# Performance work log

Hardware: AMD Instinct MI355X
Metric: run time of the kernel (lower is better)

The kernel has to match this reference:

```python
import math
import jax, jax.numpy as jnp
import numpy as np

N_NODES = 50000
N_EDGES = 600000
D = 128          # in_dim == out_dim
T = 4            # num_types
R = 4            # num_relations
H = 8            # n_heads
DK = D // H
MAX_LEN = 240    # RelTemporalEncoding max_len
EPS = 1e-5


def _sinusoid_table(n_hid, max_len):
    pos = jnp.arange(max_len, dtype=jnp.float32)[:, None]
    div = jnp.exp(jnp.arange(0, n_hid, 2, dtype=jnp.float32) * (-math.log(10000.0) / n_hid))
    s = jnp.sin(pos * div) / math.sqrt(n_hid)
    c = jnp.cos(pos * div) / math.sqrt(n_hid)
    emb = jnp.zeros((max_len, n_hid), dtype=jnp.float32)
    emb = emb.at[:, 0::2].set(s).at[:, 1::2].set(c)
    return emb


def setup_inputs() -> dict:
    key = jax.random.key(0)
    ks = jax.random.split(key, 24)
    f32 = jnp.float32
    inp = {
        'node_inp': jax.random.normal(ks[0], (N_NODES, D), dtype=f32),
        'node_type': jax.random.randint(ks[1], (N_NODES,), 0, T),
        'edge_index': jax.random.randint(ks[2], (2, N_EDGES), 0, N_NODES),
        'edge_type': jax.random.randint(ks[3], (N_EDGES,), 0, R),
        'edge_time': jax.random.randint(ks[4], (N_EDGES,), 0, MAX_LEN),
        # per-type Linear weights stored as [T, in, out] (x @ W + b)
        'Wk': jax.random.normal(ks[5], (T, D, D), dtype=f32) * 0.05,
        'bk': jnp.zeros((T, D), dtype=f32),
        'Wq': jax.random.normal(ks[6], (T, D, D), dtype=f32) * 0.05,
        'bq': jnp.zeros((T, D), dtype=f32),
        'Wv': jax.random.normal(ks[7], (T, D, D), dtype=f32) * 0.05,
        'bv': jnp.zeros((T, D), dtype=f32),
        'Wa': jax.random.normal(ks[8], (T, D, D), dtype=f32) * 0.05,
        'ba': jnp.zeros((T, D), dtype=f32),
        'gamma': jnp.ones((T, D), dtype=f32),
        'beta': jnp.zeros((T, D), dtype=f32),
        'rel_pri': jnp.ones((R, H), dtype=f32),
        'rel_att': jax.random.normal(ks[9], (R, H, DK, DK), dtype=f32) * 0.1,
        'rel_msg': jax.random.normal(ks[10], (R, H, DK, DK), dtype=f32) * 0.1,
        'skip': jnp.ones((T,), dtype=f32),
        'rte_W': jax.random.normal(ks[11], (D, D), dtype=f32) * 0.05,
        'rte_b': jnp.zeros((D,), dtype=f32),
    }
    return inp


def _type_proj(x, W, b, types):
    # all-type projection [T, N, D] then gather per-node type (T is small)
    allp = jnp.einsum('ni,tio->tno', x, W) + b[:, None, :]
    return allp[types, jnp.arange(x.shape[0])]


def reference(node_inp, node_type, edge_index, edge_type, edge_time,
              Wk, bk, Wq, bq, Wv, bv, Wa, ba, gamma, beta,
              rel_pri, rel_att, rel_msg, skip, rte_W, rte_b):
    N = node_inp.shape[0]
    E = edge_index.shape[1]
    src, tgt = edge_index[0], edge_index[1]  # j (source) -> i (target)

    # --- RelTemporalEncoding: x + Linear(emb[t]); emb is a fixed sinusoid table
    rte_out = _sinusoid_table(D, MAX_LEN) @ rte_W + rte_b  # [240, D]

    # --- per-node type-specific K/Q/V (linearity: K_t(x + rte) = K_t(x) + rte @ Wk_t)
    k_node = _type_proj(node_inp, Wk, bk, node_type)  # [N, D]
    v_node = _type_proj(node_inp, Wv, bv, node_type)
    q_node = _type_proj(node_inp, Wq, bq, node_type)
    k_rte = jnp.einsum('mi,tio->tmo', rte_out, Wk)  # [T, 240, D] (no bias; already in k_node)
    v_rte = jnp.einsum('mi,tio->tmo', rte_out, Wv)

    stype = node_type[src]
    k_e = (k_node[src] + k_rte[stype, edge_time]).reshape(E, H, DK)
    v_e = (v_node[src] + v_rte[stype, edge_time]).reshape(E, H, DK)
    q_e = q_node[tgt].reshape(E, H, DK)

    # --- per-relation head-wise transforms (R is small, fixed loop)
    k2 = jnp.zeros_like(k_e)
    msg = jnp.zeros_like(v_e)
    for r in range(R):
        sel = (edge_type == r)[:, None, None]
        k2 = jnp.where(sel, jnp.einsum('ehk,hkd->ehd', k_e, rel_att[r]), k2)
        msg = jnp.where(sel, jnp.einsum('ehk,hkd->ehd', v_e, rel_msg[r]), msg)

    logits = (q_e * k2).sum(-1) * rel_pri[edge_type] / math.sqrt(DK)  # [E, H]

    # --- softmax over edges grouped by target node
    m = jax.ops.segment_max(logits, tgt, num_segments=N)
    ex = jnp.exp(logits - m[tgt])
    den = jax.ops.segment_sum(ex, tgt, num_segments=N)
    att = ex / den[tgt]  # [E, H]

    res = (msg * att[..., None]).reshape(E, D)
    aggr = jax.ops.segment_sum(res, tgt, num_segments=N)  # [N, D]

    # --- update: per-type FFN + gated skip + per-type LayerNorm
    a = jax.nn.gelu(aggr, approximate=False)
    trans = _type_proj(a, Wa, ba, node_type)  # dropout p used in eval mode -> identity
    alpha = jax.nn.sigmoid(skip)[node_type][:, None]
    h = trans * alpha + node_inp * (1.0 - alpha)
    mu = h.mean(-1, keepdims=True)
    var = ((h - mu) ** 2).mean(-1, keepdims=True)
    out = (h - mu) / jnp.sqrt(var + EPS) * gamma[node_type] + beta[node_type]
    return out
```

## Files before the change

### kernel.cpp

```cpp
#include <hip/hip_runtime.h>
#include <math.h>

#define NH 8
#define NT 4
#define NR 4
#define MAXLEN 240

typedef __attribute__((ext_vector_type(8))) short bf16x8;
typedef __attribute__((ext_vector_type(4))) float f32x4;

__device__ __forceinline__ unsigned short f2bf(float x) {
    unsigned u = __float_as_uint(x);
    u += 0x7fffu + ((u >> 16) & 1u);
    return (unsigned short)(u >> 16);
}
__device__ __forceinline__ float bflo(unsigned u) { return __uint_as_float(u << 16); }
__device__ __forceinline__ float bfhi(unsigned u) { return __uint_as_float(u & 0xffff0000u); }
__device__ __forceinline__ unsigned pack2(float a, float b) {
    return (unsigned)f2bf(a) | ((unsigned)f2bf(b) << 16);
}
__device__ __forceinline__ float dp3(uint4 a, uint4 b, uint4 c) {
    return (bflo(a.x) + bflo(b.x)) * bflo(c.x) + (bfhi(a.x) + bfhi(b.x)) * bfhi(c.x)
         + (bflo(a.y) + bflo(b.y)) * bflo(c.y) + (bfhi(a.y) + bfhi(b.y)) * bfhi(c.y)
         + (bflo(a.z) + bflo(b.z)) * bflo(c.z) + (bfhi(a.z) + bfhi(b.z)) * bfhi(c.z)
         + (bflo(a.w) + bflo(b.w)) * bflo(c.w) + (bfhi(a.w) + bfhi(b.w)) * bfhi(c.w);
}

__global__ void zero_kernel(int* deg, int* cursor, int* dcnt, int* dcur, int N) {
    int i = blockIdx.x * blockDim.x + threadIdx.x;
    int stride = gridDim.x * blockDim.x;
    if (i < 256) { dcnt[i] = 0; dcur[i] = 0; }
    for (int j = i; j < N; j += stride) { deg[j] = 0; cursor[j] = 0; }
}

__global__ void deg_kernel(const int* __restrict__ ei, int* __restrict__ deg, int E) {
    int i = blockIdx.x * blockDim.x + threadIdx.x;
    int stride = gridDim.x * blockDim.x;
    for (int e = i; e < E; e += stride) atomicAdd(&deg[ei[E + e]], 1);
}

__global__ __launch_bounds__(256) void histA(const int* __restrict__ ntype,
                                             const int* __restrict__ deg,
                                             int* __restrict__ dcnt, int N) {
    __shared__ int h[256];
    int tid = threadIdx.x;
    h[tid] = 0;
    __syncthreads();
    int i = blockIdx.x * 256 + tid;
    if (i < N) atomicAdd(&h[ntype[i] * 64 + 63 - min(deg[i], 63)], 1);
    __syncthreads();
    if (h[tid]) atomicAdd(&dcnt[tid], h[tid]);
}

__global__ __launch_bounds__(256) void histB(const int* __restrict__ dcnt,
                                             int* __restrict__ dbase) {
    __shared__ int tmp[256];
    int v = dcnt[threadIdx.x];
    tmp[threadIdx.x] = v;
    __syncthreads();
    #pragma unroll
    for (int off = 1; off < 256; off <<= 1) {
        int t = threadIdx.x >= off ? tmp[threadIdx.x - off] : 0;
        __syncthreads();
        tmp[threadIdx.x] += t;
        __syncthreads();
    }
    dbase[threadIdx.x] = tmp[threadIdx.x] - v;
}

__global__ __launch_bounds__(256) void histC(const int* __restrict__ ntype,
                                             const int* __restrict__ deg,
                                             const int* __restrict__ dbase, int* __restrict__ dcur,
                                             int* __restrict__ nlist, int* __restrict__ spos,
                                             int* __restrict__ stype_s, int* __restrict__ deg_s,
                                             int N) {
    __shared__ int h[256];
    __shared__ int bb[256];
    __shared__ int cur[256];
    int tid = threadIdx.x;
    h[tid] = 0; cur[tid] = 0;
    __syncthreads();
    int i = blockIdx.x * 256 + tid;
    int b = -1, t = 0, dg = 0;
    if (i < N) {
        t = ntype[i]; dg = deg[i];
        b = t * 64 + 63 - min(dg, 63);
        atomicAdd(&h[b], 1);
    }
    __syncthreads();
    if (h[tid]) bb[tid] = atomicAdd(&dcur[tid], h[tid]);
    __syncthreads();
    if (i < N) {
        int r = atomicAdd(&cur[b], 1);
        int p = dbase[b] + bb[b] + r;
        nlist[p] = i;
        spos[i] = p;
        stype_s[p] = t;
        deg_s[p] = dg;
    }
}

__global__ __launch_bounds__(256) void scanA(const int* __restrict__ deg, int* __restrict__ excl,
                                             int* __restrict__ bsum, int N) {
    __shared__ int tmp[256];
    int i = blockIdx.x * 256 + threadIdx.x;
    int v = i < N ? deg[i] : 0;
    tmp[threadIdx.x] = v;
    __syncthreads();
    #pragma unroll
    for (int off = 1; off < 256; off <<= 1) {
        int t = threadIdx.x >= off ? tmp[threadIdx.x - off] : 0;
        __syncthreads();
        tmp[threadIdx.x] += t;
        __syncthreads();
    }
    if (i < N) excl[i] = tmp[threadIdx.x] - v;
    if (threadIdx.x == 255) bsum[blockIdx.x] = tmp[255];
}

__global__ __launch_bounds__(256) void scanB(int* __restrict__ bsum, int nb) {
    __shared__ int tmp[256];
    int v = threadIdx.x < nb ? bsum[threadIdx.x] : 0;
    tmp[threadIdx.x] = v;
    __syncthreads();
    #pragma unroll
    for (int off = 1; off < 256; off <<= 1) {
        int t = threadIdx.x >= off ? tmp[threadIdx.x - off] : 0;
        __syncthreads();
        tmp[threadIdx.x] += t;
        __syncthreads();
    }
    if (threadIdx.x < nb) bsum[threadIdx.x] = tmp[threadIdx.x] - v;
}

__global__ void scanC(const int* __restrict__ excl, const int* __restrict__ bsum,
                      int* __restrict__ row_start, int N) {
    int i = blockIdx.x * blockDim.x + threadIdx.x;
    if (i < N) row_start[i] = excl[i] + bsum[i >> 8];
}

__global__ void scatter_kernel(const int* __restrict__ ei, const int* __restrict__ etype,
                               const int* __restrict__ etime, const int* __restrict__ spos,
                               const int* __restrict__ dbase,
                               const int* __restrict__ row_start, int* __restrict__ cursor,
                               unsigned* __restrict__ ebuf, int E) {
    int tb1 = dbase[64], tb2 = dbase[128], tb3 = dbase[192];
    int i = blockIdx.x * blockDim.x + threadIdx.x;
    int stride = gridDim.x * blockDim.x;
    for (int e = i; e < E; e += stride) {
        int sps = spos[ei[e]];
        int spt = spos[ei[E + e]];
        int st = (sps >= tb1) + (sps >= tb2) + (sps >= tb3);
        int pos = atomicAdd(&cursor[spt], 1);
        ebuf[row_start[spt] + pos] =
            (unsigned)sps | ((unsigned)etype[e] << 17) | ((unsigned)etime[e] << 19) | ((unsigned)st << 27);
    }
}

__global__ __launch_bounds__(128) void rte_tables(
    const float* __restrict__ rte_W, const float* __restrict__ rte_b,
    const float* __restrict__ Wk, const float* __restrict__ Wv,
    const float* __restrict__ rel_msg,
    unsigned short* __restrict__ krte_bf, unsigned short* __restrict__ vmrte_bf) {
    int m = blockIdx.x, t = blockIdx.y, d = threadIdx.x;
    __shared__ float emb[128];
    __shared__ float sr[128];
    __shared__ float vr[128];
    int j2 = d & ~1;
    float div = expf((float)j2 * (-9.210340371976184f / 128.f));
    float ang = (float)m * div;
    emb[d] = ((d & 1) ? cosf(ang) : sinf(ang)) * 0.08838834764831845f;
    __syncthreads();
    float ro = rte_b[d];
    #pragma unroll 8
    for (int i = 0; i < 128; ++i) ro += emb[i] * rte_W[i * 128 + d];
    sr[d] = ro;
    __syncthreads();
    float ak = 0.f, av = 0.f;
    for (int i = 0; i < 128; ++i) {
        float rv = sr[i];
        ak += rv * Wk[(t * 128 + i) * 128 + d];
        av += rv * Wv[(t * 128 + i) * 128 + d];
    }
    krte_bf[(size_t)(t * MAXLEN + m) * 128 + d] = f2bf(ak);
    vr[d] = av;
    __syncthreads();
    int h = d >> 4, dd = d & 15;
    for (int r = 0; r < NR; ++r) {
        float acc = 0.f;
        #pragma unroll
        for (int k = 0; k < 16; ++k)
            acc += vr[h * 16 + k] * rel_msg[((r * NH + h) * 16 + k) * 16 + dd];
        vmrte_bf[(size_t)((t * 4 + r) * MAXLEN + m) * 128 + d] = f2bf(acc);
    }
}

__global__ __launch_bounds__(256) void pack_w9(
    const float* __restrict__ Wk, const float* __restrict__ Wq,
    const float* __restrict__ Wv, const float* __restrict__ Wa,
    const float* __restrict__ bk, const float* __restrict__ bq,
    const float* __restrict__ bv, const float* __restrict__ ba,
    const float* __restrict__ rel_att, const float* __restrict__ rel_msg,
    const float* __restrict__ rel_pri,
    short* __restrict__ PW2, float* __restrict__ PB) {
    if (blockIdx.x >= 320) {
        int bidx = (blockIdx.x - 320) * 256 + threadIdx.x;
        int col = bidx & 127, t = (bidx >> 7) & 3, set = bidx >> 9;
        int h = col >> 4, kk = col & 15;
        float val;
        if (set == 0) val = bk[t * 128 + col];
        else if (set == 9) val = ba[t * 128 + col];
        else if (set <= 4) {
            int r = set - 1;
            float pri = rel_pri[r * NH + h] * 0.25f;
            float acc = 0.f;
            #pragma unroll
            for (int dp = 0; dp < 16; ++dp)
                acc += bq[t * 128 + h * 16 + dp] * rel_att[((r * NH + h) * 16 + kk) * 16 + dp];
            val = acc * pri;
        } else {
            int r = set - 5;
            float acc = 0.f;
            #pragma unroll
            for (int kp = 0; kp < 16; ++kp)
                acc += bv[t * 128 + h * 16 + kp] * rel_msg[((r * NH + h) * 16 + kp) * 16 + kk];
            val = acc;
        }
        PB[bidx] = val;
        return;
    }
    int idx = blockIdx.x * 256 + threadIdx.x;
    int lane = idx & 63;
    int ks = (idx >> 6) & 3;
    int ctg = (idx >> 8) & 7;
    int t = (idx >> 11) & 3;
    int set = idx >> 13;
    int col = ctg * 16 + (lane & 15);
    int k0 = ks * 32 + (lane >> 4) * 8;
    int h = col >> 4, kk = col & 15;
    unsigned short o[8];
    if (set == 0 || set == 9) {
        const float* W = (set == 0 ? Wk : Wa) + t * 16384;
        #pragma unroll
        for (int j = 0; j < 8; ++j) o[j] = f2bf(W[(k0 + j) * 128 + col]);
    } else if (set <= 4) {
        int r = set - 1;
        float pri = rel_pri[r * NH + h] * 0.25f;
        float Ar[16];
        #pragma unroll
        for (int dp = 0; dp < 16; ++dp)
            Ar[dp] = rel_att[((r * NH + h) * 16 + kk) * 16 + dp] * pri;
        #pragma unroll
        for (int j = 0; j < 8; ++j) {
            const float* wr = Wq + (size_t)(t * 128 + k0 + j) * 128 + h * 16;
            float acc = 0.f;
            #pragma unroll
            for (int dp = 0; dp < 16; ++dp) acc += wr[dp] * Ar[dp];
            o[j] = f2bf(acc);
        }
    } else {
        int r = set - 5;
        float Mc[16];
        #pragma unroll
        for (int kp = 0; kp < 16; ++kp)
            Mc[kp] = rel_msg[((r * NH + h) * 16 + kp) * 16 + kk];
        #pragma unroll
        for (int j = 0; j < 8; ++j) {
            const float* wr = Wv + (size_t)(t * 128 + k0 + j) * 128 + h * 16;
            float acc = 0.f;
            #pragma unroll
            for (int kp = 0; kp < 16; ++kp) acc += wr[kp] * Mc[kp];
            o[j] = f2bf(acc);
        }
    }
    uint4 pk;
    pk.x = (unsigned)o[0] | ((unsigned)o[1] << 16);
    pk.y = (unsigned)o[2] | ((unsigned)o[3] << 16);
    pk.z = (unsigned)o[4] | ((unsigned)o[5] << 16);
    pk.w = (unsigned)o[6] | ((unsigned)o[7] << 16);
    *reinterpret_cast<uint4*>(PW2 + (size_t)idx * 8) = pk;
}

__global__ __launch_bounds__(256, 4) void kqv2(
    const float* __restrict__ x, const int* __restrict__ nlist_,
    const int* __restrict__ stype_s, const short* __restrict__ PW2,
    const float* __restrict__ PB,
    unsigned short* __restrict__ kn_s, unsigned short* __restrict__ qa_s,
    unsigned short* __restrict__ vm_s, int N) {
    __shared__ short af_l[2][4][64][8];
    __shared__ unsigned short ob[32][128];
    __shared__ int st_l[32];
    const int tid = threadIdx.x;
    const int sp0 = blockIdx.x * 32;
    if (tid < 32) {
        int sp = sp0 + tid;
        st_l[tid] = stype_s[sp < N ? sp : N - 1];
    }
    {
        int i = tid >> 3;
        int d0 = (tid & 7) * 16;
        int sp = sp0 + i;
        int nid = nlist_[sp < N ? sp : N - 1];
        const float* xr = x + (size_t)nid * 128 + d0;
        float4 f0 = *reinterpret_cast<const float4*>(xr);
        float4 f1 = *reinterpret_cast<const float4*>(xr + 4);
        float4 f2 = *reinterpret_cast<const float4*>(xr + 8);
        float4 f3 = *reinterpret_cast<const float4*>(xr + 12);
        int m = i >> 4, rr = i & 15;
        int ks = d0 >> 5;
        int sub = (d0 >> 3) & 3;
        uint4 p0, p1;
        p0.x = pack2(f0.x, f0.y); p0.y = pack2(f0.z, f0.w);
        p0.z = pack2(f1.x, f1.y); p0.w = pack2(f1.z, f1.w);
        p1.x = pack2(f2.x, f2.y); p1.y = pack2(f2.z, f2.w);
        p1.z = pack2(f3.x, f3.y); p1.w = pack2(f3.z, f3.w);
        *reinterpret_cast<uint4*>(&af_l[m][ks][sub * 16 + rr][0]) = p0;
        *reinterpret_cast<uint4*>(&af_l[m][ks][(sub + 1) * 16 + rr][0]) = p1;
    }
    __syncthreads();

    const int lane = tid & 63, w = tid >> 6;
    const int col_l = lane & 15, rowg = lane >> 4;
    const int t0 = st_l[0], t1 = st_l[31];

    bf16x8 afr[2][4];
    #pragma unroll
    for (int m = 0; m < 2; ++m)
        #pragma unroll
        for (int ks = 0; ks < 4; ++ks)
            afr[m][ks] = *reinterpret_cast<const bf16x8*>(&af_l[m][ks][lane][0]);

    for (int set = 0; set < 9; ++set) {
        for (int t = t0; t <= t1; ++t) {
            #pragma unroll
            for (int c = 0; c < 2; ++c) {
                int ctg = w + c * 4;
                bf16x8 pf[4];
                #pragma unroll
                for (int ks = 0; ks < 4; ++ks)
                    pf[ks] = *reinterpret_cast<const bf16x8*>(
                        PW2 + ((size_t)((((set * 4 + t) * 8 + ctg) * 4 + ks) * 64 + lane)) * 8);
                float bval = PB[(set * 4 + t) * 128 + ctg * 16 + col_l];
                #pragma unroll
                for (int m = 0; m < 2; ++m) {
                    f32x4 acc = {0.f, 0.f, 0.f, 0.f};
                    #pragma unroll
                    for (int ks = 0; ks < 4; ++ks)
                        acc = __builtin_amdgcn_mfma_f32_16x16x32_bf16(afr[m][ks], pf[ks], acc, 0, 0, 0);
                    #pragma unroll
                    for (int j = 0; j < 4; ++j) {
                        int i = m * 16 + rowg * 4 + j;
                        if (st_l[i] == t)
                            ob[i][ctg * 16 + col_l] = f2bf(acc[j] + bval);
                    }
                }
            }
        }
        __syncthreads();
        {
            int i = tid >> 3, d0 = (tid & 7) * 16;
            int sp = sp0 + i;
            if (sp < N) {
                unsigned short* dst;
                if (set == 0) dst = kn_s + (size_t)sp * 128;
                else if (set <= 4) dst = qa_s + ((size_t)sp * 4 + (set - 1)) * 128;
                else dst = vm_s + ((size_t)sp * 4 + (set - 5)) * 128;
                *reinterpret_cast<uint4*>(dst + d0) = *reinterpret_cast<const uint4*>(&ob[i][d0]);
                *reinterpret_cast<uint4*>(dst + d0 + 8) = *reinterpret_cast<const uint4*>(&ob[i][d0 + 8]);
            }
        }
        __syncthreads();
    }
}

__global__ __launch_bounds__(256) void fused_edge_attn(
    const unsigned* __restrict__ ebuf, const int* __restrict__ row_start,
    const int* __restrict__ deg_s,
    const unsigned short* __restrict__ kn_s, const unsigned short* __restrict__ krte_bf,
    const unsigned short* __restrict__ qa_s, const unsigned short* __restrict__ vm_s,
    const unsigned short* __restrict__ vmrte_bf,
    float* __restrict__ aggr, int N) {
    int sp = blockIdx.x * 16 + (threadIdx.x >> 4);
    int l16 = threadIdx.x & 15;
    if (sp >= N) return;
    uint4 q[4];
    #pragma unroll
    for (int r = 0; r < 4; ++r)
        q[r] = *reinterpret_cast<const uint4*>(qa_s + ((size_t)sp * 4 + r) * 128 + l16 * 8);
    int start = row_start[sp], cnt = deg_s[sp];
    float den = 0.f;
    float acc[8] = {0.f, 0.f, 0.f, 0.f, 0.f, 0.f, 0.f, 0.f};
    int i = 0;
    for (; i + 2 <= cnt; i += 2) {
        unsigned e0 = ebuf[start + i];
        unsigned e1 = ebuf[start + i + 1];
        int sps0 = e0 & 0x1ffff, r0 = (e0 >> 17) & 3, tm0 = (e0 >> 19) & 255, st0 = (e0 >> 27) & 3;
        int sps1 = e1 & 0x1ffff, r1 = (e1 >> 17) & 3, tm1 = (e1 >> 19) & 255, st1 = (e1 >> 27) & 3;
        uint4 kv0 = *reinterpret_cast<const uint4*>(kn_s + (size_t)sps0 * 128 + l16 * 8);
        uint4 kr0 = *reinterpret_cast<const uint4*>(krte_bf + (size_t)(st0 * MAXLEN + tm0) * 128 + l16 * 8);
        uint4 mv0 = *reinterpret_cast<const uint4*>(vm_s + ((size_t)sps0 * 4 + r0) * 128 + l16 * 8);
        uint4 mr0 = *reinterpret_cast<const uint4*>(vmrte_bf + (size_t)((st0 * 4 + r0) * MAXLEN + tm0) * 128 + l16 * 8);
        uint4 kv1 = *reinterpret_cast<const uint4*>(kn_s + (size_t)sps1 * 128 + l16 * 8);
        uint4 kr1 = *reinterpret_cast<const uint4*>(krte_bf + (size_t)(st1 * MAXLEN + tm1) * 128 + l16 * 8);
        uint4 mv1 = *reinterpret_cast<const uint4*>(vm_s + ((size_t)sps1 * 4 + r1) * 128 + l16 * 8);
        uint4 mr1 = *reinterpret_cast<const uint4*>(vmrte_bf + (size_t)((st1 * 4 + r1) * MAXLEN + tm1) * 128 + l16 * 8);
        float p0 = dp3(kv0, kr0, q[r0]);
        float p1 = dp3(kv1, kr1, q[r1]);
        p0 += __shfl_xor(p0, 1);
        p1 += __shfl_xor(p1, 1);
        float w0 = __expf(p0), w1 = __expf(p1);
        den += w0 + w1;
        acc[0] += w0 * (bflo(mv0.x) + bflo(mr0.x)) + w1 * (bflo(mv1.x) + bflo(mr1.x));
        acc[1] += w0 * (bfhi(mv0.x) + bfhi(mr0.x)) + w1 * (bfhi(mv1.x) + bfhi(mr1.x));
        acc[2] += w0 * (bflo(mv0.y) + bflo(mr0.y)) + w1 * (bflo(mv1.y) + bflo(mr1.y));
        acc[3] += w0 * (bfhi(mv0.y) + bfhi(mr0.y)) + w1 * (bfhi(mv1.y) + bfhi(mr1.y));
        acc[4] += w0 * (bflo(mv0.z) + bflo(mr0.z)) + w1 * (bflo(mv1.z) + bflo(mr1.z));
        acc[5] += w0 * (bfhi(mv0.z) + bfhi(mr0.z)) + w1 * (bfhi(mv1.z) + bfhi(mr1.z));
        acc[6] += w0 * (bflo(mv0.w) + bflo(mr0.w)) + w1 * (bflo(mv1.w) + bflo(mr1.w));
        acc[7] += w0 * (bfhi(mv0.w) + bfhi(mr0.w)) + w1 * (bfhi(mv1.w) + bfhi(mr1.w));
    }
    if (i < cnt) {
        unsigned e0 = ebuf[start + i];
        int sps0 = e0 & 0x1ffff, r0 = (e0 >> 17) & 3, tm0 = (e0 >> 19) & 255, st0 = (e0 >> 27) & 3;
        uint4 kv0 = *reinterpret_cast<const uint4*>(kn_s + (size_t)sps0 * 128 + l16 * 8);
        uint4 kr0 = *reinterpret_cast<const uint4*>(krte_bf + (size_t)(st0 * MAXLEN + tm0) * 128 + l16 * 8);
        uint4 mv0 = *reinterpret_cast<const uint4*>(vm_s + ((size_t)sps0 * 4 + r0) * 128 + l16 * 8);
        uint4 mr0 = *reinterpret_cast<const uint4*>(vmrte_bf + (size_t)((st0 * 4 + r0) * MAXLEN + tm0) * 128 + l16 * 8);
        float p0 = dp3(kv0, kr0, q[r0]);
        p0 += __shfl_xor(p0, 1);
        float w0 = __expf(p0);
        den += w0;
        acc[0] += w0 * (bflo(mv0.x) + bflo(mr0.x));
        acc[1] += w0 * (bfhi(mv0.x) + bfhi(mr0.x));
        acc[2] += w0 * (bflo(mv0.y) + bflo(mr0.y));
        acc[3] += w0 * (bfhi(mv0.y) + bfhi(mr0.y));
        acc[4] += w0 * (bflo(mv0.z) + bflo(mr0.z));
        acc[5] += w0 * (bfhi(mv0.z) + bfhi(mr0.z));
        acc[6] += w0 * (bflo(mv0.w) + bflo(mr0.w));
        acc[7] += w0 * (bfhi(mv0.w) + bfhi(mr0.w));
    }
    float inv = den > 0.f ? 1.f / den : 0.f;
    float4 o0, o1;
    o0.x = acc[0] * inv; o0.y = acc[1] * inv; o0.z = acc[2] * inv; o0.w = acc[3] * inv;
    o1.x = acc[4] * inv; o1.y = acc[5] * inv; o1.z = acc[6] * inv; o1.w = acc[7] * inv;
    float* ap = aggr + (size_t)sp * 128 + l16 * 8;
    *reinterpret_cast<float4*>(ap) = o0;
    *reinterpret_cast<float4*>(ap + 4) = o1;
}

__global__ __launch_bounds__(256, 4) void update_sorted(
    const float* __restrict__ x, const int* __restrict__ nlist_,
    const int* __restrict__ stype_s, const short* __restrict__ PW2,
    const float* __restrict__ PB, const float* __restrict__ gamma,
    const float* __restrict__ beta, const float* __restrict__ skip,
    const float* __restrict__ aggr, float* __restrict__ out, int N) {
    __shared__ short af_l[2][4][64][8];
    __shared__ float hs[32][128];
    __shared__ int st_l[32];
    __shared__ int nid_l[32];
    const int tid = threadIdx.x;
    const int sp0 = blockIdx.x * 32;
    if (tid < 32) {
        int sp = sp0 + tid;
        int spc = sp < N ? sp : N - 1;
        st_l[tid] = stype_s[spc];
        nid_l[tid] = nlist_[spc];
    }
    {
        int i = tid >> 3;
        int d0 = (tid & 7) * 16;
        int spc = sp0 + i < N ? sp0 + i : N - 1;
        const float* ar = aggr + (size_t)spc * 128 + d0;
        float g[16];
        #pragma unroll
        for (int c = 0; c < 4; ++c) {
            float4 f = *reinterpret_cast<const float4*>(ar + c * 4);
            g[c * 4 + 0] = 0.5f * f.x * (1.f + erff(f.x * 0.7071067811865476f));
            g[c * 4 + 1] = 0.5f * f.y * (1.f + erff(f.y * 0.7071067811865476f));
            g[c * 4 + 2] = 0.5f * f.z * (1.f + erff(f.z * 0.7071067811865476f));
            g[c * 4 + 3] = 0.5f * f.w * (1.f + erff(f.w * 0.7071067811865476f));
        }
        int m = i >> 4, rr = i & 15;
        int ks = d0 >> 5;
        int sub = (d0 >> 3) & 3;
        uint4 p0, p1;
        p0.x = pack2(g[0], g[1]);  p0.y = pack2(g[2], g[3]);
        p0.z = pack2(g[4], g[5]);  p0.w = pack2(g[6], g[7]);
        p1.x = pack2(g[8], g[9]);  p1.y = pack2(g[10], g[11]);
        p1.z = pack2(g[12], g[13]); p1.w = pack2(g[14], g[15]);
        *reinterpret_cast<uint4*>(&af_l[m][ks][sub * 16 + rr][0]) = p0;
        *reinterpret_cast<uint4*>(&af_l[m][ks][(sub + 1) * 16 + rr][0]) = p1;
    }
    __syncthreads();

    const int lane = tid & 63, w = tid >> 6;
    const int col_l = lane & 15, rowg = lane >> 4;
    const int t0 = st_l[0], t1 = st_l[31];

    bf16x8 afr[2][4];
    #pragma unroll
    for (int m = 0; m < 2; ++m)
        #pragma unroll
        for (int ks = 0; ks < 4; ++ks)
            afr[m][ks] = *reinterpret_cast<const bf16x8*>(&af_l[m][ks][lane][0]);

    for (int t = t0; t <= t1; ++t) {
        #pragma unroll
        for (int c = 0; c < 2; ++c) {
            int ctg = w + c * 4;
            bf16x8 pf[4];
            #pragma unroll
            for (int ks = 0; ks < 4; ++ks)
                pf[ks] = *reinterpret_cast<const bf16x8*>(
                    PW2 + ((size_t)((((9 * 4 + t) * 8 + ctg) * 4 + ks) * 64 + lane)) * 8);
            float bval = PB[(9 * 4 + t) * 128 + ctg * 16 + col_l];
            #pragma unroll
            for (int m = 0; m < 2; ++m) {
                f32x4 acc = {0.f, 0.f, 0.f, 0.f};
                #pragma unroll
                for (int ks = 0; ks < 4; ++ks)
                    acc = __builtin_amdgcn_mfma_f32_16x16x32_bf16(afr[m][ks], pf[ks], acc, 0, 0, 0);
                #pragma unroll
                for (int j = 0; j < 4; ++j) {
                    int i = m * 16 + rowg * 4 + j;
                    if (st_l[i] == t)
                        hs[i][ctg * 16 + col_l] = acc[j] + bval;
                }
            }
        }
    }
    __syncthreads();

    {
        int i = tid >> 3;
        int d0 = (tid & 7) * 16;
        int sp = sp0 + i;
        int nid = nid_l[i];
        int t = st_l[i];
        float alpha = 1.f / (1.f + expf(-skip[t]));
        const float* xr = x + (size_t)nid * 128 + d0;
        float hv[16];
        float s1 = 0.f, s2 = 0.f;
        #pragma unroll
        for (int c = 0; c < 4; ++c) {
            float4 xf = *reinterpret_cast<const float4*>(xr + c * 4);
            float4 tf;
            tf.x = hs[i][d0 + c * 4 + 0]; tf.y = hs[i][d0 + c * 4 + 1];
            tf.z = hs[i][d0 + c * 4 + 2]; tf.w = hs[i][d0 + c * 4 + 3];
            hv[c * 4 + 0] = tf.x * alpha + xf.x * (1.f - alpha);
            hv[c * 4 + 1] = tf.y * alpha + xf.y * (1.f - alpha);
            hv[c * 4 + 2] = tf.z * alpha + xf.z * (1.f - alpha);
            hv[c * 4 + 3] = tf.w * alpha + xf.w * (1.f - alpha);
            #pragma unroll
            for (int j = 0; j < 4; ++j) { s1 += hv[c * 4 + j]; s2 += hv[c * 4 + j] * hv[c * 4 + j]; }
        }
        #pragma unroll
        for (int off = 1; off < 8; off <<= 1) {
            s1 += __shfl_xor(s1, off);
            s2 += __shfl_xor(s2, off);
        }
        float mu = s1 * (1.f / 128.f);
        float var = s2 * (1.f / 128.f) - mu * mu;
        float inv = 1.f / sqrtf(var + 1e-5f);
        if (sp < N) {
            float* orow = out + (size_t)nid * 128 + d0;
            const float* gr = gamma + t * 128 + d0;
            const float* br = beta + t * 128 + d0;
            #pragma unroll
            for (int c = 0; c < 4; ++c) {
                float4 gf = *reinterpret_cast<const float4*>(gr + c * 4);
                float4 bf = *reinterpret_cast<const float4*>(br + c * 4);
                float4 of;
                of.x = (hv[c * 4 + 0] - mu) * inv * gf.x + bf.x;
                of.y = (hv[c * 4 + 1] - mu) * inv * gf.y + bf.y;
                of.z = (hv[c * 4 + 2] - mu) * inv * gf.z + bf.z;
                of.w = (hv[c * 4 + 3] - mu) * inv * gf.w + bf.w;
                *reinterpret_cast<float4*>(orow + c * 4) = of;
            }
        }
    }
}

extern "C" void kernel_launch(void* const* d_in, const int* in_sizes, int n_in,
                              void* d_out, int out_size, void* d_ws, size_t ws_size,
                              hipStream_t stream) {
    const float* node_inp = (const float*)d_in[0];
    const int*   node_type = (const int*)d_in[1];
    const int*   edge_index = (const int*)d_in[2];
    const int*   edge_type = (const int*)d_in[3];
    const int*   edge_time = (const int*)d_in[4];
    const float* Wk = (const float*)d_in[5];
    const float* bk = (const float*)d_in[6];
    const float* Wq = (const float*)d_in[7];
    const float* bq = (const float*)d_in[8];
    const float* Wv = (const float*)d_in[9];
    const float* bv = (const float*)d_in[10];
    const float* Wa = (const float*)d_in[11];
    const float* ba = (const float*)d_in[12];
    const float* gamma = (const float*)d_in[13];
    const float* beta = (const float*)d_in[14];
    const float* rel_pri = (const float*)d_in[15];
    const float* rel_att = (const float*)d_in[16];
    const float* rel_msg = (const float*)d_in[17];
    const float* skip = (const float*)d_in[18];
    const float* rte_W = (const float*)d_in[19];
    const float* rte_b = (const float*)d_in[20];

    int N = in_sizes[0] / 128;
    int E = in_sizes[3];

    char* base = (char*)d_ws;
    float* aggr = (float*)base;               base += (size_t)N * 128 * 4;
    unsigned short* kn_s = (unsigned short*)base;     base += (size_t)N * 128 * 2;
    unsigned short* qa_s = (unsigned short*)base;     base += (size_t)N * 4 * 128 * 2;
    unsigned short* vm_s = (unsigned short*)base;     base += (size_t)N * 4 * 128 * 2;
    unsigned short* krte_bf = (unsigned short*)base;  base += (size_t)NT * MAXLEN * 128 * 2;
    unsigned short* vmrte_bf = (unsigned short*)base; base += (size_t)NT * NR * MAXLEN * 128 * 2;
    short* PW2 = (short*)base;                base += (size_t)10 * NT * 128 * 128 * 2;
    float* PB = (float*)base;                 base += (size_t)10 * NT * 128 * 4;
    int* deg = (int*)base;                    base += (size_t)N * 4;
    int* deg_s = (int*)base;                  base += (size_t)N * 4;
    int* cursor = (int*)base;                 base += (size_t)N * 4;
    int* excl = (int*)base;                   base += (size_t)N * 4;
    int* row_start = (int*)base;              base += (size_t)N * 4;
    int* nlist = (int*)base;                  base += (size_t)N * 4;
    int* spos = (int*)base;                   base += (size_t)N * 4;
    int* stype_s = (int*)base;                base += (size_t)N * 4;
    int* bsum = (int*)base;                   base += 256 * 4;
    int* dcnt = (int*)base;                   base += 256 * 4;
    int* dcur = (int*)base;                   base += 256 * 4;
    int* dbase = (int*)base;                  base += 256 * 4;
    base = (char*)(((size_t)base + 15) & ~(size_t)15);
    unsigned* ebuf = (unsigned*)base;         base += (size_t)E * 4;

    int nb = (N + 255) / 256;
    int ng = (N + 255) / 256;

    zero_kernel<<<256, 256, 0, stream>>>(deg, cursor, dcnt, dcur, N);
    deg_kernel<<<1024, 256, 0, stream>>>(edge_index, deg, E);
    histA<<<ng, 256, 0, stream>>>(node_type, deg, dcnt, N);
    histB<<<1, 256, 0, stream>>>(dcnt, dbase);
    histC<<<ng, 256, 0, stream>>>(node_type, deg, dbase, dcur, nlist, spos, stype_s, deg_s, N);
    scanA<<<nb, 256, 0, stream>>>(deg_s, excl, bsum, N);
    scanB<<<1, 256, 0, stream>>>(bsum, nb);
    scanC<<<nb, 256, 0, stream>>>(excl, bsum, row_start, N);
    scatter_kernel<<<1024, 256, 0, stream>>>(edge_index, edge_type, edge_time, spos, dbase,
                                             row_start, cursor, ebuf, E);
    dim3 gt(MAXLEN, NT);
    rte_tables<<<gt, 128, 0, stream>>>(rte_W, rte_b, Wk, Wv, rel_msg, krte_bf, vmrte_bf);
    pack_w9<<<340, 256, 0, stream>>>(Wk, Wq, Wv, Wa, bk, bq, bv, ba,
                                     rel_att, rel_msg, rel_pri, PW2, PB);
    kqv2<<<(N + 31) / 32, 256, 0, stream>>>(node_inp, nlist, stype_s, PW2, PB,
                                            kn_s, qa_s, vm_s, N);
    fused_edge_attn<<<(N + 15) / 16, 256, 0, stream>>>(ebuf, row_start, deg_s,
                                                       kn_s, krte_bf, qa_s, vm_s, vmrte_bf,
                                                       aggr, N);
    update_sorted<<<(N + 31) / 32, 256, 0, stream>>>(node_inp, nlist, stype_s, PW2, PB,
                                                     gamma, beta, skip, aggr, (float*)d_out, N);
}
```

Measured before the change: 255.2 us.

## Store per-node K and V-message in scaled FP8, aggregate in bf16

Per-node key and relation-message projections are now written as custom FP8 (E4M3-like, scaled by 1/256) instead of bf16, and decoded in the edge-attention gather through half-precision bit tricks. The query bias and weights are scaled by 256 to compensate, RTE tables are scaled by 1/256, and the aggregate is stored as bf16 instead of fp32. The goal is to roughly halve the random gather traffic per edge and the aggregate write/read. In exchange, precision drops, decode costs extra ALU work, and the 2-edge unrolled loop becomes a single-edge loop.

Result: no change. 257.0 us (+0.7%).

```diff
diff --git a/kernel.cpp b/kernel.cpp
--- a/kernel.cpp
+++ b/kernel.cpp
@@ -1,4 +1,5 @@
 #include <hip/hip_runtime.h>
+#include <hip/hip_fp16.h>
 #include <math.h>
 
 #define NH 8
@@ -19,11 +20,24 @@
 __device__ __forceinline__ unsigned pack2(float a, float b) {
     return (unsigned)f2bf(a) | ((unsigned)f2bf(b) << 16);
 }
-__device__ __forceinline__ float dp3(uint4 a, uint4 b, uint4 c) {
-    return (bflo(a.x) + bflo(b.x)) * bflo(c.x) + (bfhi(a.x) + bfhi(b.x)) * bfhi(c.x)
-         + (bflo(a.y) + bflo(b.y)) * bflo(c.y) + (bfhi(a.y) + bfhi(b.y)) * bfhi(c.y)
-         + (bflo(a.z) + bflo(b.z)) * bflo(c.z) + (bfhi(a.z) + bfhi(b.z)) * bfhi(c.z)
-         + (bflo(a.w) + bflo(b.w)) * bflo(c.w) + (bfhi(a.w) + bfhi(b.w)) * bfhi(c.w);
+
+__device__ __forceinline__ void fp8x4_dec(unsigned w, float* f) {
+    unsigned ev = w & 0x00ff00ffu;
+    unsigned od = (w >> 8) & 0x00ff00ffu;
+    unsigned he = ((ev << 8) & 0x80008000u) | ((ev << 7) & 0x3f803f80u);
+    unsigned ho = ((od << 8) & 0x80008000u) | ((od << 7) & 0x3f803f80u);
+    __half2 h2e = *reinterpret_cast<__half2*>(&he);
+    __half2 h2o = *reinterpret_cast<__half2*>(&ho);
+    float2 fe = __half22float2(h2e);
+    float2 fo = __half22float2(h2o);
+    f[0] = fe.x; f[1] = fo.x; f[2] = fe.y; f[3] = fo.y;
+}
+__device__ __forceinline__ unsigned char f2fp8(float x) {
+    float cl = fminf(fmaxf(x, -448.f), 448.f);
+    __half h = __float2half(cl * 0.00390625f);
+    unsigned short hr = *reinterpret_cast<unsigned short*>(&h);
+    unsigned short rnd = (unsigned short)((hr & 0x7fff) + 0x3f + ((hr >> 7) & 1));
+    return (unsigned char)(((rnd >> 7) & 0x7f) | ((hr >> 8) & 0x80));
 }
 
 __global__ void zero_kernel(int* deg, int* cursor, int* dcnt, int* dcur, int N) {
@@ -182,7 +196,7 @@
         ak += rv * Wk[(t * 128 + i) * 128 + d];
         av += rv * Wv[(t * 128 + i) * 128 + d];
     }
-    krte_bf[(size_t)(t * MAXLEN + m) * 128 + d] = f2bf(ak);
+    krte_bf[(size_t)(t * MAXLEN + m) * 128 + d] = f2bf(ak * 0.00390625f);
     vr[d] = av;
     __syncthreads();
     int h = d >> 4, dd = d & 15;
@@ -191,7 +205,7 @@
         #pragma unroll
         for (int k = 0; k < 16; ++k)
             acc += vr[h * 16 + k] * rel_msg[((r * NH + h) * 16 + k) * 16 + dd];
-        vmrte_bf[(size_t)((t * 4 + r) * MAXLEN + m) * 128 + d] = f2bf(acc);
+        vmrte_bf[(size_t)((t * 4 + r) * MAXLEN + m) * 128 + d] = f2bf(acc * 0.00390625f);
     }
 }
 
@@ -212,7 +226,7 @@
         else if (set == 9) val = ba[t * 128 + col];
         else if (set <= 4) {
             int r = set - 1;
-            float pri = rel_pri[r * NH + h] * 0.25f;
+            float pri = rel_pri[r * NH + h] * 64.f;
             float acc = 0.f;
             #pragma unroll
             for (int dp = 0; dp < 16; ++dp)
@@ -245,7 +259,7 @@
         for (int j = 0; j < 8; ++j) o[j] = f2bf(W[(k0 + j) * 128 + col]);
     } else if (set <= 4) {
         int r = set - 1;
-        float pri = rel_pri[r * NH + h] * 0.25f;
+        float pri = rel_pri[r * NH + h] * 64.f;
         float Ar[16];
         #pragma unroll
         for (int dp = 0; dp < 16; ++dp)
@@ -285,10 +299,10 @@
     const float* __restrict__ x, const int* __restrict__ nlist_,
     const int* __restrict__ stype_s, const short* __restrict__ PW2,
     const float* __restrict__ PB,
-    unsigned short* __restrict__ kn_s, unsigned short* __restrict__ qa_s,
-    unsigned short* __restrict__ vm_s, int N) {
+    unsigned char* __restrict__ kn8, unsigned short* __restrict__ qa_s,
+    unsigned char* __restrict__ vm8, int N) {
     __shared__ short af_l[2][4][64][8];
-    __shared__ unsigned short ob[32][128];
+    __shared__ unsigned char ob8[32 * 256];
     __shared__ int st_l[32];
     const int tid = threadIdx.x;
     const int sp0 = blockIdx.x * 32;
@@ -331,6 +345,7 @@
             afr[m][ks] = *reinterpret_cast<const bf16x8*>(&af_l[m][ks][lane][0]);
 
     for (int set = 0; set < 9; ++set) {
+        bool isf8 = (set == 0 || set >= 5);
         for (int t = t0; t <= t1; ++t) {
             #pragma unroll
             for (int c = 0; c < 2; ++c) {
@@ -350,23 +365,35 @@
                     #pragma unroll
                     for (int j = 0; j < 4; ++j) {
                         int i = m * 16 + rowg * 4 + j;
-                        if (st_l[i] == t)
-                            ob[i][ctg * 16 + col_l] = f2bf(acc[j] + bval);
+                        if (st_l[i] == t) {
+                            if (isf8)
+                                ob8[i * 128 + ctg * 16 + col_l] = f2fp8(acc[j] + bval);
+                            else
+                                reinterpret_cast<unsigned short*>(ob8)[i * 128 + ctg * 16 + col_l] =
+                                    f2bf(acc[j] + bval);
+                        }
                     }
                 }
             }
         }
         __syncthreads();
-        {
+        if (isf8) {
+            int i = tid >> 3, seg = tid & 7;
+            int sp = sp0 + i;
+            if (sp < N) {
+                unsigned char* dst = (set == 0) ? (kn8 + (size_t)sp * 128)
+                                                : (vm8 + ((size_t)sp * 4 + (set - 5)) * 128);
+                *reinterpret_cast<uint4*>(dst + seg * 16) =
+                    *reinterpret_cast<const uint4*>(&ob8[i * 128 + seg * 16]);
+            }
+        } else {
             int i = tid >> 3, d0 = (tid & 7) * 16;
             int sp = sp0 + i;
             if (sp < N) {
-                unsigned short* dst;
-                if (set == 0) dst = kn_s + (size_t)sp * 128;
-                else if (set <= 4) dst = qa_s + ((size_t)sp * 4 + (set - 1)) * 128;
-                else dst = vm_s + ((size_t)sp * 4 + (set - 5)) * 128;
-                *reinterpret_cast<uint4*>(dst + d0) = *reinterpret_cast<const uint4*>(&ob[i][d0]);
-                *reinterpret_cast<uint4*>(dst + d0 + 8) = *reinterpret_cast<const uint4*>(&ob[i][d0 + 8]);
+                unsigned short* dst = qa_s + ((size_t)sp * 4 + (set - 1)) * 128;
+                const unsigned short* src = reinterpret_cast<const unsigned short*>(ob8) + i * 128 + d0;
+                *reinterpret_cast<uint4*>(dst + d0) = *reinterpret_cast<const uint4*>(src);
+                *reinterpret_cast<uint4*>(dst + d0 + 8) = *reinterpret_cast<const uint4*>(src + 8);
             }
         }
         __syncthreads();
@@ -376,10 +403,10 @@
 __global__ __launch_bounds__(256) void fused_edge_attn(
     const unsigned* __restrict__ ebuf, const int* __restrict__ row_start,
     const int* __restrict__ deg_s,
-    const unsigned short* __restrict__ kn_s, const unsigned short* __restrict__ krte_bf,
-    const unsigned short* __restrict__ qa_s, const unsigned short* __restrict__ vm_s,
+    const unsigned char* __restrict__ kn8, const unsigned short* __restrict__ krte_bf,
+    const unsigned short* __restrict__ qa_s, const unsigned char* __restrict__ vm8,
     const unsigned short* __restrict__ vmrte_bf,
-    float* __restrict__ aggr, int N) {
+    unsigned short* __restrict__ aggr_bf, int N) {
     int sp = blockIdx.x * 16 + (threadIdx.x >> 4);
     int l16 = threadIdx.x & 15;
     if (sp >= N) return;
@@ -390,62 +417,40 @@
     int start = row_start[sp], cnt = deg_s[sp];
     float den = 0.f;
     float acc[8] = {0.f, 0.f, 0.f, 0.f, 0.f, 0.f, 0.f, 0.f};
-    int i = 0;
-    for (; i + 2 <= cnt; i += 2) {
-        unsigned e0 = ebuf[start + i];
-        unsigned e1 = ebuf[start + i + 1];
-        int sps0 = e0 & 0x1ffff, r0 = (e0 >> 17) & 3, tm0 = (e0 >> 19) & 255, st0 = (e0 >> 27) & 3;
-        int sps1 = e1 & 0x1ffff, r1 = (e1 >> 17) & 3, tm1 = (e1 >> 19) & 255, st1 = (e1 >> 27) & 3;
-        uint4 kv0 = *reinterpret_cast<const uint4*>(kn_s + (size_t)sps0 * 128 + l16 * 8);
-        uint4 kr0 = *reinterpret_cast<const uint4*>(krte_bf + (size_t)(st0 * MAXLEN + tm0) * 128 + l16 * 8);
-        uint4 mv0 = *reinterpret_cast<const uint4*>(vm_s + ((size_t)sps0 * 4 + r0) * 128 + l16 * 8);
-        uint4 mr0 = *reinterpret_cast<const uint4*>(vmrte_bf + (size_t)((st0 * 4 + r0) * MAXLEN + tm0) * 128 + l16 * 8);
-        uint4 kv1 = *reinterpret_cast<const uint4*>(kn_s + (size_t)sps1 * 128 + l16 * 8);
-        uint4 kr1 = *reinterpret_cast<const uint4*>(krte_bf + (size_t)(st1 * MAXLEN + tm1) * 128 + l16 * 8);
-        uint4 mv1 = *reinterpret_cast<const uint4*>(vm_s + ((size_t)sps1 * 4 + r1) * 128 + l16 * 8);
-        uint4 mr1 = *reinterpret_cast<const uint4*>(vmrte_bf + (size_t)((st1 * 4 + r1) * MAXLEN + tm1) * 128 + l16 * 8);
-        float p0 = dp3(kv0, kr0, q[r0]);
-        float p1 = dp3(kv1, kr1, q[r1]);
-        p0 += __shfl_xor(p0, 1);
-        p1 += __shfl_xor(p1, 1);
-        float w0 = __expf(p0), w1 = __expf(p1);
-        den += w0 + w1;
-        acc[0] += w0 * (bflo(mv0.x) + bflo(mr0.x)) + w1 * (bflo(mv1.x) + bflo(mr1.x));
-        acc[1] += w0 * (bfhi(mv0.x) + bfhi(mr0.x)) + w1 * (bfhi(mv1.x) + bfhi(mr1.x));
-        acc[2] += w0 * (bflo(mv0.y) + bflo(mr0.y)) + w1 * (bflo(mv1.y) + bflo(mr1.y));
-        acc[3] += w0 * (bfhi(mv0.y) + bfhi(mr0.y)) + w1 * (bfhi(mv1.y) + bfhi(mr1.y));
-        acc[4] += w0 * (bflo(mv0.z) + bflo(mr0.z)) + w1 * (bflo(mv1.z) + bflo(mr1.z));
-        acc[5] += w0 * (bfhi(mv0.z) + bfhi(mr0.z)) + w1 * (bfhi(mv1.z) + bfhi(mr1.z));
-        acc[6] += w0 * (bflo(mv0.w) + bflo(mr0.w)) + w1 * (bflo(mv1.w) + bflo(mr1.w));
-        acc[7] += w0 * (bfhi(mv0.w) + bfhi(mr0.w)) + w1 * (bfhi(mv1.w) + bfhi(mr1.w));
-    }
-    if (i < cnt) {
+    for (int i = 0; i < cnt; ++i) {
         unsigned e0 = ebuf[start + i];
         int sps0 = e0 & 0x1ffff, r0 = (e0 >> 17) & 3, tm0 = (e0 >> 19) & 255, st0 = (e0 >> 27) & 3;
-        uint4 kv0 = *reinterpret_cast<const uint4*>(kn_s + (size_t)sps0 * 128 + l16 * 8);
-        uint4 kr0 = *reinterpret_cast<const uint4*>(krte_bf + (size_t)(st0 * MAXLEN + tm0) * 128 + l16 * 8);
-        uint4 mv0 = *reinterpret_cast<const uint4*>(vm_s + ((size_t)sps0 * 4 + r0) * 128 + l16 * 8);
-        uint4 mr0 = *reinterpret_cast<const uint4*>(vmrte_bf + (size_t)((st0 * 4 + r0) * MAXLEN + tm0) * 128 + l16 * 8);
-        float p0 = dp3(kv0, kr0, q[r0]);
-        p0 += __shfl_xor(p0, 1);
-        float w0 = __expf(p0);
+        uint2 kv = *reinterpret_cast<const uint2*>(kn8 + (size_t)sps0 * 128 + l16 * 8);
+        uint4 kr = *reinterpret_cast<const uint4*>(krte_bf + (size_t)(st0 * MAXLEN + tm0) * 128 + l16 * 8);
+        uint2 mv = *reinterpret_cast<const uint2*>(vm8 + ((size_t)sps0 * 4 + r0) * 128 + l16 * 8);
+        uint4 mr = *reinterpret_cast<const uint4*>(vmrte_bf + (size_t)((st0 * 4 + r0) * MAXLEN + tm0) * 128 + l16 * 8);
+        uint4 qr = q[r0];
+        float kf[8], mf[8];
+        fp8x4_dec(kv.x, kf); fp8x4_dec(kv.y, kf + 4);
+        fp8x4_dec(mv.x, mf); fp8x4_dec(mv.y, mf + 4);
+        float p = (kf[0] + bflo(kr.x)) * bflo(qr.x) + (kf[1] + bfhi(kr.x)) * bfhi(qr.x)
+                + (kf[2] + bflo(kr.y)) * bflo(qr.y) + (kf[3] + bfhi(kr.y)) * bfhi(qr.y)
+                + (kf[4] + bflo(kr.z)) * bflo(qr.z) + (kf[5] + bfhi(kr.z)) * bfhi(qr.z)
+                + (kf[6] + bflo(kr.w)) * bflo(qr.w) + (kf[7] + bfhi(kr.w)) * bfhi(qr.w);
+        p += __shfl_xor(p, 1);
+        float w0 = __expf(p);
         den += w0;
-        acc[0] += w0 * (bflo(mv0.x) + bflo(mr0.x));
-        acc[1] += w0 * (bfhi(mv0.x) + bfhi(mr0.x));
-        acc[2] += w0 * (bflo(mv0.y) + bflo(mr0.y));
-        acc[3] += w0 * (bfhi(mv0.y) + bfhi(mr0.y));
-        acc[4] += w0 * (bflo(mv0.z) + bflo(mr0.z));
-        acc[5] += w0 * (bfhi(mv0.z) + bfhi(mr0.z));
-        acc[6] += w0 * (bflo(mv0.w) + bflo(mr0.w));
-        acc[7] += w0 * (bfhi(mv0.w) + bfhi(mr0.w));
-    }
-    float inv = den > 0.f ? 1.f / den : 0.f;
-    float4 o0, o1;
-    o0.x = acc[0] * inv; o0.y = acc[1] * inv; o0.z = acc[2] * inv; o0.w = acc[3] * inv;
-    o1.x = acc[4] * inv; o1.y = acc[5] * inv; o1.z = acc[6] * inv; o1.w = acc[7] * inv;
-    float* ap = aggr + (size_t)sp * 128 + l16 * 8;
-    *reinterpret_cast<float4*>(ap) = o0;
-    *reinterpret_cast<float4*>(ap + 4) = o1;
+        acc[0] += w0 * (mf[0] + bflo(mr.x));
+        acc[1] += w0 * (mf[1] + bfhi(mr.x));
+        acc[2] += w0 * (mf[2] + bflo(mr.y));
+        acc[3] += w0 * (mf[3] + bfhi(mr.y));
+        acc[4] += w0 * (mf[4] + bflo(mr.z));
+        acc[5] += w0 * (mf[5] + bfhi(mr.z));
+        acc[6] += w0 * (mf[6] + bflo(mr.w));
+        acc[7] += w0 * (mf[7] + bfhi(mr.w));
+    }
+    float inv = den > 0.f ? 256.f / den : 0.f;
+    uint4 o;
+    o.x = pack2(acc[0] * inv, acc[1] * inv);
+    o.y = pack2(acc[2] * inv, acc[3] * inv);
+    o.z = pack2(acc[4] * inv, acc[5] * inv);
+    o.w = pack2(acc[6] * inv, acc[7] * inv);
+    *reinterpret_cast<uint4*>(aggr_bf + (size_t)sp * 128 + l16 * 8) = o;
 }
 
 __global__ __launch_bounds__(256, 4) void update_sorted(
@@ -453,7 +458,7 @@
     const int* __restrict__ stype_s, const short* __restrict__ PW2,
     const float* __restrict__ PB, const float* __restrict__ gamma,
     const float* __restrict__ beta, const float* __restrict__ skip,
-    const float* __restrict__ aggr, float* __restrict__ out, int N) {
+    const unsigned short* __restrict__ aggr_bf, float* __restrict__ out, int N) {
     __shared__ short af_l[2][4][64][8];
     __shared__ float hs[32][128];
     __shared__ int st_l[32];
@@ -470,15 +475,16 @@
         int i = tid >> 3;
         int d0 = (tid & 7) * 16;
         int spc = sp0 + i < N ? sp0 + i : N - 1;
-        const float* ar = aggr + (size_t)spc * 128 + d0;
+        const unsigned short* ar = aggr_bf + (size_t)spc * 128 + d0;
+        uint4 v0 = *reinterpret_cast<const uint4*>(ar);
+        uint4 v1 = *reinterpret_cast<const uint4*>(ar + 8);
+        unsigned vv[8] = {v0.x, v0.y, v0.z, v0.w, v1.x, v1.y, v1.z, v1.w};
         float g[16];
         #pragma unroll
-        for (int c = 0; c < 4; ++c) {
-            float4 f = *reinterpret_cast<const float4*>(ar + c * 4);
-            g[c * 4 + 0] = 0.5f * f.x * (1.f + erff(f.x * 0.7071067811865476f));
-            g[c * 4 + 1] = 0.5f * f.y * (1.f + erff(f.y * 0.7071067811865476f));
-            g[c * 4 + 2] = 0.5f * f.z * (1.f + erff(f.z * 0.7071067811865476f));
-            g[c * 4 + 3] = 0.5f * f.w * (1.f + erff(f.w * 0.7071067811865476f));
+        for (int c = 0; c < 8; ++c) {
+            float a0 = bflo(vv[c]), a1 = bfhi(vv[c]);
+            g[c * 2 + 0] = 0.5f * a0 * (1.f + erff(a0 * 0.7071067811865476f));
+            g[c * 2 + 1] = 0.5f * a1 * (1.f + erff(a1 * 0.7071067811865476f));
         }
         int m = i >> 4, rr = i & 15;
         int ks = d0 >> 5;
@@ -610,10 +616,10 @@
     int E = in_sizes[3];
 
     char* base = (char*)d_ws;
-    float* aggr = (float*)base;               base += (size_t)N * 128 * 4;
-    unsigned short* kn_s = (unsigned short*)base;     base += (size_t)N * 128 * 2;
+    unsigned short* aggr_bf = (unsigned short*)base;  base += (size_t)N * 128 * 2;
+    unsigned char* kn8 = (unsigned char*)base;        base += (size_t)N * 128;
+    unsigned char* vm8 = (unsigned char*)base;        base += (size_t)N * 4 * 128;
     unsigned short* qa_s = (unsigned short*)base;     base += (size_t)N * 4 * 128 * 2;
-    unsigned short* vm_s = (unsigned short*)base;     base += (size_t)N * 4 * 128 * 2;
     unsigned short* krte_bf = (unsigned short*)base;  base += (size_t)NT * MAXLEN * 128 * 2;
     unsigned short* vmrte_bf = (unsigned short*)base; base += (size_t)NT * NR * MAXLEN * 128 * 2;
     short* PW2 = (short*)base;                base += (size_t)10 * NT * 128 * 128 * 2;
@@ -651,10 +657,10 @@
     pack_w9<<<340, 256, 0, stream>>>(Wk, Wq, Wv, Wa, bk, bq, bv, ba,
                                      rel_att, rel_msg, rel_pri, PW2, PB);
     kqv2<<<(N + 31) / 32, 256, 0, stream>>>(node_inp, nlist, stype_s, PW2, PB,
-                                            kn_s, qa_s, vm_s, N);
+                                            kn8, qa_s, vm8, N);
     fused_edge_attn<<<(N + 15) / 16, 256, 0, stream>>>(ebuf, row_start, deg_s,
-                                                       kn_s, krte_bf, qa_s, vm_s, vmrte_bf,
-                                                       aggr, N);
+                                                       kn8, krte_bf, qa_s, vm8, vmrte_bf,
+                                                       aggr_bf, N);
     update_sorted<<<(N + 31) / 32, 256, 0, stream>>>(node_inp, nlist, stype_s, PW2, PB,
-                                                     gamma, beta, skip, aggr, (float*)d_out, N);
-}
+                                                     gamma, beta, skip, aggr_bf, (float*)d_out, N);
+}
```
